# Kernel optimization log

Measured on AMD Instinct MI355X. Metric: run time of the kernel, lower is better.

## Reference

```python
import jax, jax.numpy as jnp
import numpy as np

E = 8        # num_local_experts
H = 1024     # hidden_dim
F = 4096     # intermediate_dim
T = 16384    # total permuted tokens (sum of tokens_per_expert)


def setup_inputs() -> dict:
    key = jax.random.key(0)
    k_x, k_w1, k_w2 = jax.random.split(key, 3)
    x = jax.random.normal(k_x, (T, H), dtype=jnp.float32)
    # Ragged tokens-per-expert summing exactly to T (variable group sizes).
    rng = np.random.default_rng(0)
    bounds = np.sort(rng.integers(0, T, size=E - 1))
    counts = np.diff(np.concatenate([[0], bounds, [T]])).astype(np.int32)
    tokens_per_expert = jnp.asarray(counts)  # [E], int32, sums to T
    # xavier_normal_ init per expert matrix: std = sqrt(2/(fan_in+fan_out))
    std = (2.0 / (H + F)) ** 0.5
    weight1 = jax.random.normal(k_w1, (E, H, F), dtype=jnp.float32) * std  # fc1
    weight2 = jax.random.normal(k_w2, (E, F, H), dtype=jnp.float32) * std  # fc2
    return {
        "permuted_local_hidden_states": x,
        "weight1": weight1,
        "weight2": weight2,
        "tokens_per_expert": tokens_per_expert,
    }


def reference(permuted_local_hidden_states, weight1, weight2, tokens_per_expert):
    # Grouped GEMM: rows of x are grouped contiguously by expert; group e uses
    # weight[e]. lax.ragged_dot is the exact analogue of gg.ops.gmm(trans_b=False).
    fc1 = jax.lax.ragged_dot(permuted_local_hidden_states, weight1,
                             tokens_per_expert)            # [T, F]
    act = jax.nn.gelu(fc1, approximate=False)               # activation fused between GEMMs
    fc2 = jax.lax.ragged_dot(act, weight2, tokens_per_expert)  # [T, H]
    return fc2
```

## Files before the change

### kernel.cpp

```cpp
#include <hip/hip_runtime.h>
#include <hip/hip_bf16.h>

#define E_NUM 8
#define H_DIM 1024
#define F_DIM 4096
#define T_TOK 16384

#define NT 256
#define MT_MAX (T_TOK / 128 + E_NUM)
#define MT256 (T_TOK / 256 + E_NUM)

typedef __attribute__((ext_vector_type(8))) short bf16x8;
typedef __attribute__((ext_vector_type(4))) float f32x4;

__device__ __forceinline__ short f2bf(float f) {
    unsigned u = __builtin_bit_cast(unsigned, f);
    u += 0x7FFFu + ((u >> 16) & 1u);
    return (short)(u >> 16);
}

__device__ __forceinline__ float exp2_fast(float a) {
#if __has_builtin(__builtin_amdgcn_exp2f)
    return __builtin_amdgcn_exp2f(a);
#else
    return exp2f(a);
#endif
}
__device__ __forceinline__ float rcp_fast(float a) {
#if __has_builtin(__builtin_amdgcn_rcpf)
    return __builtin_amdgcn_rcpf(a);
#else
    return 1.0f / a;
#endif
}

__device__ __forceinline__ float fast_gelu(float x) {
    float x2 = x * x;
    float y = x * (0.7978845608f + 0.0356774081f * x2);
    float z = exp2_fast(y * 2.8853900817779268f);
    float r = rcp_fast(z + 1.0f);
    return x * (1.0f - r);
}

__device__ __forceinline__ void gload16(const void* g, void* l) {
    __builtin_amdgcn_global_load_lds(
        (const __attribute__((address_space(1))) void*)g,
        (__attribute__((address_space(3))) void*)l, 16, 0, 0);
}

template<int N>
__device__ __forceinline__ void vmwait() {
    if constexpr (N == 0) asm volatile("s_waitcnt vmcnt(0)" ::: "memory");
    else if constexpr (N == 1) asm volatile("s_waitcnt vmcnt(1)" ::: "memory");
    else if constexpr (N == 2) asm volatile("s_waitcnt vmcnt(2)" ::: "memory");
    else if constexpr (N == 3) asm volatile("s_waitcnt vmcnt(3)" ::: "memory");
    else if constexpr (N == 4) asm volatile("s_waitcnt vmcnt(4)" ::: "memory");
}

__device__ __forceinline__ void bar() {
    asm volatile("s_barrier" ::: "memory");
}

__device__ __forceinline__ void tile_map128(const int* __restrict__ cnt, int mt,
                                            int& row0, int& rend, int& e_out) {
    int acc = 0, off = 0;
    e_out = -1;
    for (int i = 0; i < E_NUM; ++i) {
        int c = cnt[i];
        int nti = (c + 127) >> 7;
        if (mt < acc + nti) {
            e_out = i; row0 = off + (mt - acc) * 128; rend = off + c; return;
        }
        acc += nti; off += c;
    }
}

__device__ __forceinline__ void tile_map256(const int* __restrict__ cnt, int mt,
                                            int& row0, int& rend, int& e_out) {
    int acc = 0, off = 0;
    e_out = -1;
    for (int i = 0; i < E_NUM; ++i) {
        int c = cnt[i];
        int nti = (c + 255) >> 8;
        if (mt < acc + nti) {
            e_out = i; row0 = off + (mt - acc) * 256; rend = off + c; return;
        }
        acc += nti; off += c;
    }
}

__global__ __launch_bounds__(NT)
void cvt_x_kernel(const float* __restrict__ in, short* __restrict__ out, int n8) {
    int i = blockIdx.x * blockDim.x + threadIdx.x;
    const int stride = gridDim.x * blockDim.x;
    for (; i < n8; i += stride) {
        f32x4 f0 = ((const f32x4*)in)[(size_t)i * 2];
        f32x4 f1 = ((const f32x4*)in)[(size_t)i * 2 + 1];
        bf16x8 v;
        v[0] = f2bf(f0[0]); v[1] = f2bf(f0[1]); v[2] = f2bf(f0[2]); v[3] = f2bf(f0[3]);
        v[4] = f2bf(f1[0]); v[5] = f2bf(f1[1]); v[6] = f2bf(f1[2]); v[7] = f2bf(f1[3]);
        ((bf16x8*)out)[i] = v;
    }
}

__global__ __launch_bounds__(NT)
void transpose_cvt(const float* __restrict__ in, short* __restrict__ out,
                   int R, int C) {
    __shared__ short tb[64][72];
    const int e = blockIdx.z;
    const float* ine = in + (size_t)e * R * C;
    short* oute = out + (size_t)e * R * C;
    const int c0 = blockIdx.x * 64, r0 = blockIdx.y * 64;
    const int t = threadIdx.x;
    const int rl = t >> 4, cl = (t & 15) * 4;
#pragma unroll
    for (int p = 0; p < 4; ++p) {
        int r = rl + p * 16;
        f32x4 f = *(const f32x4*)(ine + (size_t)(r0 + r) * C + c0 + cl);
#pragma unroll
        for (int j = 0; j < 4; ++j) tb[cl + j][r] = f2bf(f[j]);
    }
    __syncthreads();
    const int c2 = t >> 3, rc = (t & 7) * 8;
#pragma unroll
    for (int p = 0; p < 2; ++p) {
        int c = c2 + p * 32;
        bf16x8 v = *(const bf16x8*)&tb[c][rc];
        *(bf16x8*)(oute + (size_t)(c0 + c) * R + r0 + rc) = v;
    }
}

#define G8P_READ_A(mh)                                                        \
    _Pragma("unroll") for (int f = 0; f < MF / 2; ++f) {                      \
        const int r_ = ((mh) * (MF / 2) + f) * (16 * WM) + wm * 16 + lr;      \
        _Pragma("unroll") for (int kk = 0; kk < 2; ++kk) {                    \
            const int u_ = (r_ * 8 + kk * 4 + lg) ^ (r_ & 7);                 \
            areg[f][kk] = ((const bf16x8*)Ac)[u_];                            \
        }                                                                     \
    }

#define G8P_READ_B(nh)                                                        \
    _Pragma("unroll") for (int g = 0; g < NF / 2; ++g) {                      \
        const int r_ = ((nh) * (NF / 2) + g) * (16 * WN) + wn * 16 + lr;      \
        _Pragma("unroll") for (int kk = 0; kk < 2; ++kk) {                    \
            const int u_ = (r_ * 8 + kk * 4 + lg) ^ (r_ & 7);                 \
            breg[(nh) * (NF / 2) + g][kk] = ((const bf16x8*)Bc)[u_];          \
        }                                                                     \
    }

#define G8P_QUAD(mh, nh)                                                      \
    _Pragma("unroll") for (int f = 0; f < MF / 2; ++f)                        \
    _Pragma("unroll") for (int g = 0; g < NF / 2; ++g)                        \
    _Pragma("unroll") for (int kk = 0; kk < 2; ++kk)                          \
        acc[(mh) * (MF / 2) + f][(nh) * (NF / 2) + g] =                       \
            __builtin_amdgcn_mfma_f32_16x16x32_bf16(                          \
                areg[f][kk], breg[(nh) * (NF / 2) + g][kk],                   \
                acc[(mh) * (MF / 2) + f][(nh) * (NF / 2) + g], 0, 0, 0);

template<int BN, int WM, int WN, bool GELU, int LDC, int NTX, int KTOT>
__global__ __launch_bounds__(512, 2)
void gemm8p(const short* __restrict__ A, const short* __restrict__ Bw,
            const int* __restrict__ cnt, void* __restrict__ Cout) {
    constexpr int MF = 256 / WM / 16;
    constexpr int NF = BN / WN / 16;
    constexpr int B_P = BN / 64;
    constexpr int A_SH = 16384;
    constexpr int SEG = (256 + BN) * 64;
    constexpr int KT = KTOT / 64;
    constexpr int VM_END = (B_P == 4) ? 4 : 3;

    __shared__ __align__(16) short lds[2 * SEG];

    const int lin = blockIdx.x;
    constexpr int CPX = (NTX * MT256) / 8;
    const int wg = (lin & 7) * CPX + (lin >> 3);
    const int mt = wg / NTX;
    const int nt = wg - mt * NTX;

    int row0, rend, e;
    tile_map256(cnt, mt, row0, rend, e);
    if (e < 0) return;
    const int n0 = nt * BN;
    const short* Be = Bw + (size_t)e * ((size_t)F_DIM * H_DIM);

    const int tid = threadIdx.x;
    const int lane = tid & 63;
    const int lr = lane & 15;
    const int lg = lane >> 4;
    const int w = tid >> 6;
    const int wm = w / WN;
    const int wn = w % WN;

    const short* ag[4];
    const short* bg[B_P];
#pragma unroll
    for (int p = 0; p < 4; ++p) {
        int s = p * 512 + tid;
        int r = s >> 3;
        int kc = (s & 7) ^ (r & 7);
        int grow = row0 + r;
        if (grow >= T_TOK) grow = T_TOK - 1;
        ag[p] = A + (size_t)grow * KTOT + kc * 8;
    }
#pragma unroll
    for (int p = 0; p < B_P; ++p) {
        int s = p * 512 + tid;
        int r = s >> 3;
        int kc = (s & 7) ^ (r & 7);
        bg[p] = Be + (size_t)(n0 + r) * KTOT + kc * 8;
    }

    f32x4 acc[MF][NF];
#pragma unroll
    for (int i = 0; i < MF; ++i)
#pragma unroll
        for (int j = 0; j < NF; ++j) acc[i][j] = (f32x4){0.f, 0.f, 0.f, 0.f};
    bf16x8 areg[MF / 2][2];
    bf16x8 breg[NF][2];

    {
        short* An = lds;
        short* Bn = lds + A_SH;
        gload16(ag[0], An + (0 * 512 + tid) * 8); ag[0] += 64;
        gload16(ag[1], An + (1 * 512 + tid) * 8); ag[1] += 64;
        gload16(bg[0], Bn + (0 * 512 + tid) * 8); bg[0] += 64;
        if constexpr (B_P == 4) { gload16(bg[1], Bn + (1 * 512 + tid) * 8); bg[1] += 64; }
        gload16(ag[2], An + (2 * 512 + tid) * 8); ag[2] += 64;
        gload16(ag[3], An + (3 * 512 + tid) * 8); ag[3] += 64;
        if constexpr (B_P == 4) {
            gload16(bg[2], Bn + (2 * 512 + tid) * 8); bg[2] += 64;
            gload16(bg[3], Bn + (3 * 512 + tid) * 8); bg[3] += 64;
        } else {
            gload16(bg[1], Bn + (1 * 512 + tid) * 8); bg[1] += 64;
        }
    }
    vmwait<VM_END>();
    bar();

    int cur = 0;
    for (int kt = 0; kt < KT - 1; ++kt) {
        const short* Ac = lds + cur * SEG;
        const short* Bc = Ac + A_SH;
        short* An = lds + (cur ^ 1) * SEG;
        short* Bn = An + A_SH;

        G8P_READ_A(0)
        G8P_READ_B(0)
        gload16(ag[0], An + (0 * 512 + tid) * 8); ag[0] += 64;
        gload16(ag[1], An + (1 * 512 + tid) * 8); ag[1] += 64;
        bar();
        __builtin_amdgcn_s_setprio(1);
        G8P_QUAD(0, 0)
        __builtin_amdgcn_s_setprio(0);

        vmwait<2>();
        bar();
        G8P_READ_B(1)
        gload16(bg[0], Bn + (0 * 512 + tid) * 8); bg[0] += 64;
        if constexpr (B_P == 4) { gload16(bg[1], Bn + (1 * 512 + tid) * 8); bg[1] += 64; }
        bar();
        __builtin_amdgcn_s_setprio(1);
        G8P_QUAD(0, 1)
        __builtin_amdgcn_s_setprio(0);

        G8P_READ_A(1)
        gload16(ag[2], An + (2 * 512 + tid) * 8); ag[2] += 64;
        gload16(ag[3], An + (3 * 512 + tid) * 8); ag[3] += 64;
        bar();
        __builtin_amdgcn_s_setprio(1);
        G8P_QUAD(1, 1)
        __builtin_amdgcn_s_setprio(0);

        if constexpr (B_P == 4) {
            gload16(bg[2], Bn + (2 * 512 + tid) * 8); bg[2] += 64;
            gload16(bg[3], Bn + (3 * 512 + tid) * 8); bg[3] += 64;
        } else {
            gload16(bg[1], Bn + (1 * 512 + tid) * 8); bg[1] += 64;
        }
        bar();
        __builtin_amdgcn_s_setprio(1);
        G8P_QUAD(1, 0)
        __builtin_amdgcn_s_setprio(0);
        vmwait<VM_END>();
        bar();
        cur ^= 1;
    }

    {
        const short* Ac = lds + cur * SEG;
        const short* Bc = Ac + A_SH;
        G8P_READ_A(0)
        G8P_READ_B(0)
        G8P_QUAD(0, 0)
        vmwait<0>();
        bar();
        G8P_READ_B(1)
        G8P_QUAD(0, 1)
        G8P_READ_A(1)
        G8P_QUAD(1, 1)
        G8P_QUAD(1, 0)
    }

#pragma unroll
    for (int f = 0; f < MF; ++f) {
#pragma unroll
        for (int g = 0; g < NF; ++g) {
            const int gcol = n0 + g * (16 * WN) + wn * 16 + lr;
#pragma unroll
            for (int rr = 0; rr < 4; ++rr) {
                const int grow = row0 + f * (16 * WM) + wm * 16 + lg * 4 + rr;
                if (grow < rend) {
                    float v = acc[f][g][rr];
                    if constexpr (GELU) {
                        ((short*)Cout)[(size_t)grow * LDC + gcol] = f2bf(fast_gelu(v));
                    } else {
                        ((float*)Cout)[(size_t)grow * LDC + gcol] = v;
                    }
                }
            }
        }
    }
}

__global__ __launch_bounds__(NT)
void gemm1_kernel(const float* __restrict__ X, const float* __restrict__ W1,
                  const int* __restrict__ cnt, short* __restrict__ act) {
    __shared__ short Alds[128 * 64];
    __shared__ short Blds[128 * 64];

    int row0, rend, e;
    tile_map128(cnt, blockIdx.y, row0, rend, e);
    if (e < 0) return;

    const int n0 = blockIdx.x * 128;
    const float* W = W1 + (size_t)e * H_DIM * F_DIM;

    const int tid = threadIdx.x;
    const int lane = tid & 63;
    const int w = tid >> 6;
    const int wr = (w >> 1) * 64;
    const int wc = (w & 1) * 64;
    const int lr = lane & 15;
    const int lg = lane >> 4;

    const int a_r0 = tid >> 3;
    const int a_kc = tid & 7;
    const int b_n = tid & 127;
    const int b_kg = (tid >> 7) * 8;

    f32x4 acc[4][4];
#pragma unroll
    for (int i = 0; i < 4; ++i)
#pragma unroll
        for (int j = 0; j < 4; ++j) acc[i][j] = (f32x4){0.f, 0.f, 0.f, 0.f};

    for (int kt = 0; kt < H_DIM / 64; ++kt) {
        const int k0 = kt * 64;
#pragma unroll
        for (int p = 0; p < 4; ++p) {
            int r = a_r0 + 32 * p;
            int grow = row0 + r;
            if (grow > T_TOK - 1) grow = T_TOK - 1;
            const float* src = X + (size_t)grow * H_DIM + k0 + a_kc * 8;
            f32x4 f0 = *(const f32x4*)src;
            f32x4 f1 = *(const f32x4*)(src + 4);
            bf16x8 v;
            v[0] = f2bf(f0[0]); v[1] = f2bf(f0[1]); v[2] = f2bf(f0[2]); v[3] = f2bf(f0[3]);
            v[4] = f2bf(f1[0]); v[5] = f2bf(f1[1]); v[6] = f2bf(f1[2]); v[7] = f2bf(f1[3]);
            ((bf16x8*)Alds)[(r * 8 + a_kc) ^ (r & 7)] = v;
        }
#pragma unroll
        for (int p = 0; p < 4; ++p) {
            int kb = p * 16 + b_kg;
            const float* src = W + (size_t)(k0 + kb) * F_DIM + n0 + b_n;
            bf16x8 v;
#pragma unroll
            for (int j = 0; j < 8; ++j) v[j] = f2bf(src[(size_t)j * F_DIM]);
            ((bf16x8*)Blds)[(b_n * 8 + (kb >> 3)) ^ (b_n & 7)] = v;
        }
        __syncthreads();
#pragma unroll
        for (int kk = 0; kk < 2; ++kk) {
            bf16x8 af[4], bfr[4];
#pragma unroll
            for (int fm = 0; fm < 4; ++fm) {
                int r = wr + fm * 16 + lr;
                af[fm] = ((bf16x8*)Alds)[(r * 8 + kk * 4 + lg) ^ (r & 7)];
            }
#pragma unroll
            for (int fn = 0; fn < 4; ++fn) {
                int n = wc + fn * 16 + lr;
                bfr[fn] = ((bf16x8*)Blds)[(n * 8 + kk * 4 + lg) ^ (n & 7)];
            }
#pragma unroll
            for (int fm = 0; fm < 4; ++fm)
#pragma unroll
                for (int fn = 0; fn < 4; ++fn)
                    acc[fm][fn] = __builtin_amdgcn_mfma_f32_16x16x32_bf16(
                        af[fm], bfr[fn], acc[fm][fn], 0, 0, 0);
        }
        __syncthreads();
    }

#pragma unroll
    for (int fm = 0; fm < 4; ++fm)
#pragma unroll
        for (int fn = 0; fn < 4; ++fn) {
            int gcol = n0 + wc + fn * 16 + lr;
#pragma unroll
            for (int rr = 0; rr < 4; ++rr) {
                int grow = row0 + wr + fm * 16 + lg * 4 + rr;
                if (grow < rend)
                    act[(size_t)grow * F_DIM + gcol] = f2bf(fast_gelu(acc[fm][fn][rr]));
            }
        }
}

__global__ __launch_bounds__(NT)
void gemm2_kernel(const short* __restrict__ ACT, const float* __restrict__ W2,
                  const int* __restrict__ cnt, float* __restrict__ out) {
    __shared__ short Alds[128 * 64];
    __shared__ short Blds[128 * 64];

    int row0, rend, e;
    tile_map128(cnt, blockIdx.y, row0, rend, e);
    if (e < 0) return;

    const int n0 = blockIdx.x * 128;
    const float* W = W2 + (size_t)e * F_DIM * H_DIM;

    const int tid = threadIdx.x;
    const int lane = tid & 63;
    const int w = tid >> 6;
    const int wr = (w >> 1) * 64;
    const int wc = (w & 1) * 64;
    const int lr = lane & 15;
    const int lg = lane >> 4;

    const int a_r0 = tid >> 3;
    const int a_kc = tid & 7;
    const int b_n = tid & 127;
    const int b_kg = (tid >> 7) * 8;

    f32x4 acc[4][4];
#pragma unroll
    for (int i = 0; i < 4; ++i)
#pragma unroll
        for (int j = 0; j < 4; ++j) acc[i][j] = (f32x4){0.f, 0.f, 0.f, 0.f};

    for (int kt = 0; kt < F_DIM / 64; ++kt) {
        const int k0 = kt * 64;
#pragma unroll
        for (int p = 0; p < 4; ++p) {
            int r = a_r0 + 32 * p;
            int grow = row0 + r;
            if (grow > T_TOK - 1) grow = T_TOK - 1;
            bf16x8 v = *(const bf16x8*)(ACT + (size_t)grow * F_DIM + k0 + a_kc * 8);
            ((bf16x8*)Alds)[(r * 8 + a_kc) ^ (r & 7)] = v;
        }
#pragma unroll
        for (int p = 0; p < 4; ++p) {
            int kb = p * 16 + b_kg;
            const float* src = W + (size_t)(k0 + kb) * H_DIM + n0 + b_n;
            bf16x8 v;
#pragma unroll
            for (int j = 0; j < 8; ++j) v[j] = f2bf(src[(size_t)j * H_DIM]);
            ((bf16x8*)Blds)[(b_n * 8 + (kb >> 3)) ^ (b_n & 7)] = v;
        }
        __syncthreads();
#pragma unroll
        for (int kk = 0; kk < 2; ++kk) {
            bf16x8 af[4], bfr[4];
#pragma unroll
            for (int fm = 0; fm < 4; ++fm) {
                int r = wr + fm * 16 + lr;
                af[fm] = ((bf16x8*)Alds)[(r * 8 + kk * 4 + lg) ^ (r & 7)];
            }
#pragma unroll
            for (int fn = 0; fn < 4; ++fn) {
                int n = wc + fn * 16 + lr;
                bfr[fn] = ((bf16x8*)Blds)[(n * 8 + kk * 4 + lg) ^ (n & 7)];
            }
#pragma unroll
            for (int fm = 0; fm < 4; ++fm)
#pragma unroll
                for (int fn = 0; fn < 4; ++fn)
                    acc[fm][fn] = __builtin_amdgcn_mfma_f32_16x16x32_bf16(
                        af[fm], bfr[fn], acc[fm][fn], 0, 0, 0);
        }
        __syncthreads();
    }

#pragma unroll
    for (int fm = 0; fm < 4; ++fm)
#pragma unroll
        for (int fn = 0; fn < 4; ++fn) {
            int gcol = n0 + wc + fn * 16 + lr;
#pragma unroll
            for (int rr = 0; rr < 4; ++rr) {
                int grow = row0 + wr + fm * 16 + lg * 4 + rr;
                if (grow < rend) out[(size_t)grow * H_DIM + gcol] = acc[fm][fn][rr];
            }
        }
}

extern "C" void kernel_launch(void* const* d_in, const int* in_sizes, int n_in,
                              void* d_out, int out_size, void* d_ws, size_t ws_size,
                              hipStream_t stream) {
    const float* x  = (const float*)d_in[0];
    const float* w1 = (const float*)d_in[1];
    const float* w2 = (const float*)d_in[2];
    const int* cnt  = (const int*)d_in[3];
    float* out = (float*)d_out;

    const size_t ACT_B = (size_t)T_TOK * F_DIM * 2;
    const size_t WT_B  = (size_t)E_NUM * F_DIM * H_DIM * 2;
    const size_t XB_B  = (size_t)T_TOK * H_DIM * 2;

    if (ws_size >= ACT_B + WT_B + XB_B) {
        short* act = (short*)d_ws;
        short* wt  = (short*)((char*)d_ws + ACT_B);
        short* xb  = (short*)((char*)d_ws + ACT_B + WT_B);

        cvt_x_kernel<<<2048, NT, 0, stream>>>(x, xb, T_TOK * H_DIM / 8);
        transpose_cvt<<<dim3(F_DIM / 64, H_DIM / 64, E_NUM), NT, 0, stream>>>(
            w1, wt, H_DIM, F_DIM);
        gemm8p<256, 2, 4, true, F_DIM, 16, H_DIM>
            <<<16 * MT256, 512, 0, stream>>>(xb, wt, cnt, (void*)act);
        transpose_cvt<<<dim3(H_DIM / 64, F_DIM / 64, E_NUM), NT, 0, stream>>>(
            w2, wt, F_DIM, H_DIM);
        gemm8p<128, 4, 2, false, H_DIM, 8, F_DIM>
            <<<8 * MT256, 512, 0, stream>>>(act, wt, cnt, (void*)out);
    } else if (ws_size >= ACT_B) {
        short* act = (short*)d_ws;
        gemm1_kernel<<<dim3(F_DIM / 128, MT_MAX), NT, 0, stream>>>(x, w1, cnt, act);
        gemm2_kernel<<<dim3(H_DIM / 128, MT_MAX), NT, 0, stream>>>(act, w2, cnt, out);
    }
}
```

Baseline: 486.5 us.

## Specialize grouped GEMM to 256x256 tiles and trim pipeline barriers

The templated gemm8p kernel is hard-wired to a 256x256 output tile with a 2x4 wave layout, so the second GEMM (fc2) now uses 256-wide N tiles instead of 128 and launches half as many blocks. The main loop's wait and barrier points are rearranged: one mid-iteration barrier and the end-of-iteration wait and barrier are removed. Each half of the next stage's loads is now awaited just before the MFMA quad that consumes it. This is meant to improve weight reuse in fc2 and cut synchronization stalls. The cost is fewer blocks for fc2, with lower occupancy and possible load imbalance across CUs, and larger LDS use per block.

Measured after the change: 475.3 us. 2.3% less time.

```diff
diff --git a/kernel.cpp b/kernel.cpp
--- a/kernel.cpp
+++ b/kernel.cpp
@@ -131,8 +131,8 @@
 }
 
 #define G8P_READ_A(mh)                                                        \
-    _Pragma("unroll") for (int f = 0; f < MF / 2; ++f) {                      \
-        const int r_ = ((mh) * (MF / 2) + f) * (16 * WM) + wm * 16 + lr;      \
+    _Pragma("unroll") for (int f = 0; f < 4; ++f) {                           \
+        const int r_ = ((mh) * 4 + f) * 32 + wm * 16 + lr;                    \
         _Pragma("unroll") for (int kk = 0; kk < 2; ++kk) {                    \
             const int u_ = (r_ * 8 + kk * 4 + lg) ^ (r_ & 7);                 \
             areg[f][kk] = ((const bf16x8*)Ac)[u_];                            \
@@ -140,34 +140,30 @@
     }
 
 #define G8P_READ_B(nh)                                                        \
-    _Pragma("unroll") for (int g = 0; g < NF / 2; ++g) {                      \
-        const int r_ = ((nh) * (NF / 2) + g) * (16 * WN) + wn * 16 + lr;      \
+    _Pragma("unroll") for (int g = 0; g < 2; ++g) {                           \
+        const int r_ = ((nh) * 2 + g) * 64 + wn * 16 + lr;                    \
         _Pragma("unroll") for (int kk = 0; kk < 2; ++kk) {                    \
             const int u_ = (r_ * 8 + kk * 4 + lg) ^ (r_ & 7);                 \
-            breg[(nh) * (NF / 2) + g][kk] = ((const bf16x8*)Bc)[u_];          \
+            breg[nh][g][kk] = ((const bf16x8*)Bc)[u_];                        \
         }                                                                     \
     }
 
 #define G8P_QUAD(mh, nh)                                                      \
-    _Pragma("unroll") for (int f = 0; f < MF / 2; ++f)                        \
-    _Pragma("unroll") for (int g = 0; g < NF / 2; ++g)                        \
+    _Pragma("unroll") for (int f = 0; f < 4; ++f)                             \
+    _Pragma("unroll") for (int g = 0; g < 2; ++g)                             \
     _Pragma("unroll") for (int kk = 0; kk < 2; ++kk)                          \
-        acc[(mh) * (MF / 2) + f][(nh) * (NF / 2) + g] =                       \
+        acc[(mh) * 4 + f][(nh) * 2 + g] =                                     \
             __builtin_amdgcn_mfma_f32_16x16x32_bf16(                          \
-                areg[f][kk], breg[(nh) * (NF / 2) + g][kk],                   \
-                acc[(mh) * (MF / 2) + f][(nh) * (NF / 2) + g], 0, 0, 0);
-
-template<int BN, int WM, int WN, bool GELU, int LDC, int NTX, int KTOT>
+                areg[f][kk], breg[nh][g][kk],                                 \
+                acc[(mh) * 4 + f][(nh) * 2 + g], 0, 0, 0);
+
+template<bool GELU, int LDC, int NTX, int KTOT>
 __global__ __launch_bounds__(512, 2)
 void gemm8p(const short* __restrict__ A, const short* __restrict__ Bw,
             const int* __restrict__ cnt, void* __restrict__ Cout) {
-    constexpr int MF = 256 / WM / 16;
-    constexpr int NF = BN / WN / 16;
-    constexpr int B_P = BN / 64;
     constexpr int A_SH = 16384;
-    constexpr int SEG = (256 + BN) * 64;
+    constexpr int SEG = 32768;
     constexpr int KT = KTOT / 64;
-    constexpr int VM_END = (B_P == 4) ? 4 : 3;
 
     __shared__ __align__(16) short lds[2 * SEG];
 
@@ -180,7 +176,7 @@
     int row0, rend, e;
     tile_map256(cnt, mt, row0, rend, e);
     if (e < 0) return;
-    const int n0 = nt * BN;
+    const int n0 = nt * 256;
     const short* Be = Bw + (size_t)e * ((size_t)F_DIM * H_DIM);
 
     const int tid = threadIdx.x;
@@ -188,11 +184,11 @@
     const int lr = lane & 15;
     const int lg = lane >> 4;
     const int w = tid >> 6;
-    const int wm = w / WN;
-    const int wn = w % WN;
+    const int wm = w >> 2;
+    const int wn = w & 3;
 
     const short* ag[4];
-    const short* bg[B_P];
+    const short* bg[4];
 #pragma unroll
     for (int p = 0; p < 4; ++p) {
         int s = p * 512 + tid;
@@ -201,22 +197,16 @@
         int grow = row0 + r;
         if (grow >= T_TOK) grow = T_TOK - 1;
         ag[p] = A + (size_t)grow * KTOT + kc * 8;
-    }
-#pragma unroll
-    for (int p = 0; p < B_P; ++p) {
-        int s = p * 512 + tid;
-        int r = s >> 3;
-        int kc = (s & 7) ^ (r & 7);
         bg[p] = Be + (size_t)(n0 + r) * KTOT + kc * 8;
     }
 
-    f32x4 acc[MF][NF];
-#pragma unroll
-    for (int i = 0; i < MF; ++i)
-#pragma unroll
-        for (int j = 0; j < NF; ++j) acc[i][j] = (f32x4){0.f, 0.f, 0.f, 0.f};
-    bf16x8 areg[MF / 2][2];
-    bf16x8 breg[NF][2];
+    f32x4 acc[8][4];
+#pragma unroll
+    for (int i = 0; i < 8; ++i)
+#pragma unroll
+        for (int j = 0; j < 4; ++j) acc[i][j] = (f32x4){0.f, 0.f, 0.f, 0.f};
+    bf16x8 areg[4][2];
+    bf16x8 breg[2][2][2];
 
     {
         short* An = lds;
@@ -224,17 +214,13 @@
         gload16(ag[0], An + (0 * 512 + tid) * 8); ag[0] += 64;
         gload16(ag[1], An + (1 * 512 + tid) * 8); ag[1] += 64;
         gload16(bg[0], Bn + (0 * 512 + tid) * 8); bg[0] += 64;
-        if constexpr (B_P == 4) { gload16(bg[1], Bn + (1 * 512 + tid) * 8); bg[1] += 64; }
+        gload16(bg[1], Bn + (1 * 512 + tid) * 8); bg[1] += 64;
         gload16(ag[2], An + (2 * 512 + tid) * 8); ag[2] += 64;
         gload16(ag[3], An + (3 * 512 + tid) * 8); ag[3] += 64;
-        if constexpr (B_P == 4) {
-            gload16(bg[2], Bn + (2 * 512 + tid) * 8); bg[2] += 64;
-            gload16(bg[3], Bn + (3 * 512 + tid) * 8); bg[3] += 64;
-        } else {
-            gload16(bg[1], Bn + (1 * 512 + tid) * 8); bg[1] += 64;
-        }
-    }
-    vmwait<VM_END>();
+        gload16(bg[2], Bn + (2 * 512 + tid) * 8); bg[2] += 64;
+        gload16(bg[3], Bn + (3 * 512 + tid) * 8); bg[3] += 64;
+    }
+    vmwait<4>();
     bar();
 
     int cur = 0;
@@ -248,16 +234,15 @@
         G8P_READ_B(0)
         gload16(ag[0], An + (0 * 512 + tid) * 8); ag[0] += 64;
         gload16(ag[1], An + (1 * 512 + tid) * 8); ag[1] += 64;
+        vmwait<2>();
         bar();
         __builtin_amdgcn_s_setprio(1);
         G8P_QUAD(0, 0)
         __builtin_amdgcn_s_setprio(0);
 
-        vmwait<2>();
-        bar();
         G8P_READ_B(1)
         gload16(bg[0], Bn + (0 * 512 + tid) * 8); bg[0] += 64;
-        if constexpr (B_P == 4) { gload16(bg[1], Bn + (1 * 512 + tid) * 8); bg[1] += 64; }
+        gload16(bg[1], Bn + (1 * 512 + tid) * 8); bg[1] += 64;
         bar();
         __builtin_amdgcn_s_setprio(1);
         G8P_QUAD(0, 1)
@@ -271,18 +256,13 @@
         G8P_QUAD(1, 1)
         __builtin_amdgcn_s_setprio(0);
 
-        if constexpr (B_P == 4) {
-            gload16(bg[2], Bn + (2 * 512 + tid) * 8); bg[2] += 64;
-            gload16(bg[3], Bn + (3 * 512 + tid) * 8); bg[3] += 64;
-        } else {
-            gload16(bg[1], Bn + (1 * 512 + tid) * 8); bg[1] += 64;
-        }
+        gload16(bg[2], Bn + (2 * 512 + tid) * 8); bg[2] += 64;
+        gload16(bg[3], Bn + (3 * 512 + tid) * 8); bg[3] += 64;
+        vmwait<4>();
         bar();
         __builtin_amdgcn_s_setprio(1);
         G8P_QUAD(1, 0)
         __builtin_amdgcn_s_setprio(0);
-        vmwait<VM_END>();
-        bar();
         cur ^= 1;
     }
 
@@ -302,13 +282,13 @@
     }
 
 #pragma unroll
-    for (int f = 0; f < MF; ++f) {
-#pragma unroll
-        for (int g = 0; g < NF; ++g) {
-            const int gcol = n0 + g * (16 * WN) + wn * 16 + lr;
+    for (int f = 0; f < 8; ++f) {
+#pragma unroll
+        for (int g = 0; g < 4; ++g) {
+            const int gcol = n0 + g * 64 + wn * 16 + lr;
 #pragma unroll
             for (int rr = 0; rr < 4; ++rr) {
-                const int grow = row0 + f * (16 * WM) + wm * 16 + lg * 4 + rr;
+                const int grow = row0 + f * 32 + wm * 16 + lg * 4 + rr;
                 if (grow < rend) {
                     float v = acc[f][g][rr];
                     if constexpr (GELU) {
@@ -525,12 +505,12 @@
         cvt_x_kernel<<<2048, NT, 0, stream>>>(x, xb, T_TOK * H_DIM / 8);
         transpose_cvt<<<dim3(F_DIM / 64, H_DIM / 64, E_NUM), NT, 0, stream>>>(
             w1, wt, H_DIM, F_DIM);
-        gemm8p<256, 2, 4, true, F_DIM, 16, H_DIM>
+        gemm8p<true, F_DIM, 16, H_DIM>
             <<<16 * MT256, 512, 0, stream>>>(xb, wt, cnt, (void*)act);
         transpose_cvt<<<dim3(H_DIM / 64, F_DIM / 64, E_NUM), NT, 0, stream>>>(
             w2, wt, F_DIM, H_DIM);
-        gemm8p<128, 4, 2, false, H_DIM, 8, F_DIM>
-            <<<8 * MT256, 512, 0, stream>>>(act, wt, cnt, (void*)out);
+        gemm8p<false, H_DIM, 4, F_DIM>
+            <<<4 * MT256, 512, 0, stream>>>(act, wt, cnt, (void*)out);
     } else if (ws_size >= ACT_B) {
         short* act = (short*)d_ws;
         gemm1_kernel<<<dim3(F_DIM / 128, MT_MAX), NT, 0, stream>>>(x, w1, cnt, act);
```
